# Optimization experiments

Hardware: AMD Instinct MI355X
Metric: run time of the kernel (lower is better)

Reference implementation:

```python
import jax, jax.numpy as jnp
import numpy as np

N_ITERS = 21
TEMPERATURE = 0.01


def setup_inputs() -> dict:
    key = jax.random.key(0)
    input_tensor = jax.random.normal(key, (65536, 1296), dtype=jnp.float32)
    return {"input_tensor": input_tensor}


def reference(input_tensor) -> jnp.ndarray:
    n = input_tensor.shape[1]
    m = n // 36  # 36: side length of the permutation matrix
    log_alpha = input_tensor.reshape(-1, m, m) / TEMPERATURE  # [B, 36, 36]
    # 21 Sinkhorn iterations: alternate row / column log-normalization.
    # Same math as log(sum(exp(.))) in the torch source, written stably.
    for _ in range(N_ITERS):
        log_alpha = log_alpha - jax.nn.logsumexp(log_alpha, axis=2, keepdims=True)
        log_alpha = log_alpha - jax.nn.logsumexp(log_alpha, axis=1, keepdims=True)
    return jnp.exp(log_alpha)
```

## Files before the change

kernel.cpp:

```cpp
#include <hip/hip_runtime.h>

#define SCALE 144.269504088896340736f

template <int CTRL>
__device__ __forceinline__ float dppf(float x) {
    return __builtin_bit_cast(
        float, __builtin_amdgcn_update_dpp(0, __builtin_bit_cast(int, x),
                                           CTRL, 0xF, 0xF, true));
}

__device__ __forceinline__ float qsum(float x) {
    x += dppf<0x39>(x);
    x += dppf<0x4E>(x);
    return x;
}
__device__ __forceinline__ float qmax(float x) {
    x = fmaxf(x, dppf<0x39>(x));
    x = fmaxf(x, dppf<0x4E>(x));
    return x;
}
__device__ __forceinline__ float asum(float x) {
    x += dppf<0x124>(x);
    x += dppf<0x128>(x);
    return x;
}
__device__ __forceinline__ float amax(float x) {
    x = fmaxf(x, dppf<0x124>(x));
    x = fmaxf(x, dppf<0x128>(x));
    return x;
}

typedef float f32x4 __attribute__((ext_vector_type(4)));

__device__ __forceinline__ f32x4 load4u(const float* p) {
    f32x4 v;
    __builtin_memcpy(&v, p, 16);
    return v;
}
__device__ __forceinline__ void store4u(float* p, f32x4 v) {
    __builtin_memcpy(p, &v, 16);
}

__global__ __launch_bounds__(256, 3) void sinkhorn_kernel(
    const float* __restrict__ in, float* __restrict__ out) {
    const int lane = threadIdx.x & 63;
    const int wv   = threadIdx.x >> 6;
    const int q    = lane >> 4;
    const int a    = (lane >> 2) & 3;
    const int b    = lane & 3;
    const int m    = blockIdx.x * 16 + wv * 4 + q;

    const float* src = in  + (size_t)m * 1296 + (a * 9) * 36 + b * 9;
    float*       dst = out + (size_t)m * 1296 + (a * 9) * 36 + b * 9;

    float C[81];
    #pragma unroll
    for (int r = 0; r < 9; ++r) {
        f32x4 v0 = load4u(src + r * 36);
        f32x4 v1 = load4u(src + r * 36 + 4);
        #pragma unroll
        for (int s = 0; s < 4; ++s) C[r * 9 + s] = v0[s];
        #pragma unroll
        for (int s = 0; s < 4; ++s) C[r * 9 + 4 + s] = v1[s];
        C[r * 9 + 8] = src[r * 36 + 8];
    }

    float a2s[9], u[9], w[9];
    #pragma unroll
    for (int r = 0; r < 9; ++r) {
        float mx = C[r * 9];
        #pragma unroll
        for (int s = 1; s < 9; ++s) mx = fmaxf(mx, C[r * 9 + s]);
        a2s[r] = qmax(mx) * SCALE;
    }

    #pragma unroll
    for (int r = 0; r < 9; ++r) {
        float acc = 0.f;
        #pragma unroll
        for (int s = 0; s < 9; ++s)
            acc += __builtin_amdgcn_exp2f(
                __builtin_fmaf(C[r * 9 + s], SCALE, -a2s[r]));
        u[r] = __builtin_amdgcn_rcpf(qsum(acc));
    }

    float b2s[9];
    #pragma unroll
    for (int s = 0; s < 9; ++s) {
        float mx = __builtin_fmaf(C[s], SCALE, -a2s[0]);
        #pragma unroll
        for (int r = 1; r < 9; ++r)
            mx = fmaxf(mx, __builtin_fmaf(C[r * 9 + s], SCALE, -a2s[r]));
        b2s[s] = amax(mx);
    }

    #pragma unroll
    for (int r = 0; r < 9; ++r)
        #pragma unroll
        for (int s = 0; s < 9; ++s)
            C[r * 9 + s] = __builtin_amdgcn_exp2f(
                __builtin_fmaf(C[r * 9 + s], SCALE, -a2s[r]) - b2s[s]);

    #pragma unroll
    for (int s = 0; s < 9; ++s) {
        float acc = 0.f;
        #pragma unroll
        for (int r = 0; r < 9; ++r) acc = fmaf(C[r * 9 + s], u[r], acc);
        w[s] = __builtin_amdgcn_rcpf(asum(acc));
    }

    #pragma unroll 1
    for (int it = 0; it < 20; ++it) {
        #pragma unroll
        for (int r = 0; r < 9; ++r) {
            float acc = 0.f;
            #pragma unroll
            for (int s = 0; s < 9; ++s) acc = fmaf(C[r * 9 + s], w[s], acc);
            u[r] = __builtin_amdgcn_rcpf(qsum(acc));
        }
        #pragma unroll
        for (int s = 0; s < 9; ++s) {
            float acc = 0.f;
            #pragma unroll
            for (int r = 0; r < 9; ++r) acc = fmaf(C[r * 9 + s], u[r], acc);
            w[s] = __builtin_amdgcn_rcpf(asum(acc));
        }
    }

    #pragma unroll
    for (int r = 0; r < 9; ++r) {
        const float ur = u[r];
        float p[9];
        #pragma unroll
        for (int s = 0; s < 9; ++s) p[s] = C[r * 9 + s] * ur * w[s];
        f32x4 v0, v1;
        #pragma unroll
        for (int s = 0; s < 4; ++s) v0[s] = p[s];
        #pragma unroll
        for (int s = 0; s < 4; ++s) v1[s] = p[4 + s];
        store4u(dst + r * 36, v0);
        store4u(dst + r * 36 + 4, v1);
        dst[r * 36 + 8] = p[8];
    }
}

extern "C" void kernel_launch(void* const* d_in, const int* in_sizes, int n_in,
                              void* d_out, int out_size, void* d_ws, size_t ws_size,
                              hipStream_t stream) {
    const float* in  = (const float*)d_in[0];
    float*       out = (float*)d_out;
    sinkhorn_kernel<<<dim3(4096), dim3(256), 0, stream>>>(in, out);
}
```

Measured before the change: 575.8 us.

## Pack Sinkhorn matvecs into float2 ops and reorder initial normalisation

Stores the per-thread 9x9 block as eight float2 columns plus one scalar column so the repeated row and column matvecs can use packed FP32 multiply/FMA (v_pk_fma_f32) on CDNA. The setup is also reordered: the column max is taken first, the kernel is exponentiated once, and the first row normaliser is folded in by scaling with exp2 of the column max. This drops the separate exp pass per row. The risk is extra register pressure or scalarisation if the compiler does not emit packed instructions, and a slightly different numerical path for the first normalisation.

```diff
diff --git a/kernel.cpp b/kernel.cpp
--- a/kernel.cpp
+++ b/kernel.cpp
@@ -1,6 +1,9 @@
 #include <hip/hip_runtime.h>
 
 #define SCALE 144.269504088896340736f
+
+typedef float f32x2 __attribute__((ext_vector_type(2)));
+typedef float f32x4 __attribute__((ext_vector_type(4)));
 
 template <int CTRL>
 __device__ __forceinline__ float dppf(float x) {
@@ -30,8 +33,6 @@
     return x;
 }
 
-typedef float f32x4 __attribute__((ext_vector_type(4)));
-
 __device__ __forceinline__ f32x4 load4u(const float* p) {
     f32x4 v;
     __builtin_memcpy(&v, p, 16);
@@ -53,94 +54,138 @@
     const float* src = in  + (size_t)m * 1296 + (a * 9) * 36 + b * 9;
     float*       dst = out + (size_t)m * 1296 + (a * 9) * 36 + b * 9;
 
-    float C[81];
+    f32x2 C2[9][4];
+    float C8[9];
     #pragma unroll
     for (int r = 0; r < 9; ++r) {
         f32x4 v0 = load4u(src + r * 36);
         f32x4 v1 = load4u(src + r * 36 + 4);
-        #pragma unroll
-        for (int s = 0; s < 4; ++s) C[r * 9 + s] = v0[s];
-        #pragma unroll
-        for (int s = 0; s < 4; ++s) C[r * 9 + 4 + s] = v1[s];
-        C[r * 9 + 8] = src[r * 36 + 8];
+        C2[r][0] = f32x2{v0.x, v0.y};
+        C2[r][1] = f32x2{v0.z, v0.w};
+        C2[r][2] = f32x2{v1.x, v1.y};
+        C2[r][3] = f32x2{v1.z, v1.w};
+        C8[r] = src[r * 36 + 8];
     }
 
-    float a2s[9], u[9], w[9];
+    float a2s[9];
     #pragma unroll
     for (int r = 0; r < 9; ++r) {
-        float mx = C[r * 9];
+        float mx = C8[r];
         #pragma unroll
-        for (int s = 1; s < 9; ++s) mx = fmaxf(mx, C[r * 9 + s]);
+        for (int p = 0; p < 4; ++p)
+            mx = fmaxf(mx, fmaxf(C2[r][p].x, C2[r][p].y));
         a2s[r] = qmax(mx) * SCALE;
+    }
+
+    const f32x2 S2 = {SCALE, SCALE};
+    #pragma unroll
+    for (int r = 0; r < 9; ++r) {
+        const f32x2 a2p = {a2s[r], a2s[r]};
+        #pragma unroll
+        for (int p = 0; p < 4; ++p) C2[r][p] = C2[r][p] * S2 - a2p;
+        C8[r] = __builtin_fmaf(C8[r], SCALE, -a2s[r]);
+    }
+
+    f32x2 b22[4];
+    float b28;
+    #pragma unroll
+    for (int p = 0; p < 4; ++p) {
+        f32x2 mx = C2[0][p];
+        #pragma unroll
+        for (int r = 1; r < 9; ++r) {
+            mx.x = fmaxf(mx.x, C2[r][p].x);
+            mx.y = fmaxf(mx.y, C2[r][p].y);
+        }
+        b22[p] = f32x2{amax(mx.x), amax(mx.y)};
+    }
+    {
+        float mx = C8[0];
+        #pragma unroll
+        for (int r = 1; r < 9; ++r) mx = fmaxf(mx, C8[r]);
+        b28 = amax(mx);
     }
 
     #pragma unroll
     for (int r = 0; r < 9; ++r) {
-        float acc = 0.f;
         #pragma unroll
-        for (int s = 0; s < 9; ++s)
-            acc += __builtin_amdgcn_exp2f(
-                __builtin_fmaf(C[r * 9 + s], SCALE, -a2s[r]));
-        u[r] = __builtin_amdgcn_rcpf(qsum(acc));
+        for (int p = 0; p < 4; ++p) {
+            const f32x2 e = C2[r][p] - b22[p];
+            C2[r][p].x = __builtin_amdgcn_exp2f(e.x);
+            C2[r][p].y = __builtin_amdgcn_exp2f(e.y);
+        }
+        C8[r] = __builtin_amdgcn_exp2f(C8[r] - b28);
     }
 
-    float b2s[9];
-    #pragma unroll
-    for (int s = 0; s < 9; ++s) {
-        float mx = __builtin_fmaf(C[s], SCALE, -a2s[0]);
+    f32x2 u2[9];
+    {
+        f32x2 t2[4];
         #pragma unroll
-        for (int r = 1; r < 9; ++r)
-            mx = fmaxf(mx, __builtin_fmaf(C[r * 9 + s], SCALE, -a2s[r]));
-        b2s[s] = amax(mx);
+        for (int p = 0; p < 4; ++p)
+            t2[p] = f32x2{__builtin_amdgcn_exp2f(b22[p].x),
+                          __builtin_amdgcn_exp2f(b22[p].y)};
+        const float t8 = __builtin_amdgcn_exp2f(b28);
+        #pragma unroll
+        for (int r = 0; r < 9; ++r) {
+            f32x2 acc2 = C2[r][0] * t2[0];
+            #pragma unroll
+            for (int p = 1; p < 4; ++p) acc2 += C2[r][p] * t2[p];
+            const float acc = __builtin_fmaf(C8[r], t8, acc2.x) + acc2.y;
+            const float ur = __builtin_amdgcn_rcpf(qsum(acc));
+            u2[r] = f32x2{ur, ur};
+        }
     }
 
-    #pragma unroll
-    for (int r = 0; r < 9; ++r)
+    f32x2 w2[4];
+    float w8;
+
+    auto col_step = [&]() {
+        f32x2 acc[4];
         #pragma unroll
-        for (int s = 0; s < 9; ++s)
-            C[r * 9 + s] = __builtin_amdgcn_exp2f(
-                __builtin_fmaf(C[r * 9 + s], SCALE, -a2s[r]) - b2s[s]);
+        for (int p = 0; p < 4; ++p) acc[p] = C2[0][p] * u2[0];
+        float acc8 = C8[0] * u2[0].x;
+        #pragma unroll
+        for (int r = 1; r < 9; ++r) {
+            #pragma unroll
+            for (int p = 0; p < 4; ++p) acc[p] += C2[r][p] * u2[r];
+            acc8 = __builtin_fmaf(C8[r], u2[r].x, acc8);
+        }
+        #pragma unroll
+        for (int p = 0; p < 4; ++p)
+            w2[p] = f32x2{__builtin_amdgcn_rcpf(asum(acc[p].x)),
+                          __builtin_amdgcn_rcpf(asum(acc[p].y))};
+        w8 = __builtin_amdgcn_rcpf(asum(acc8));
+    };
 
-    #pragma unroll
-    for (int s = 0; s < 9; ++s) {
-        float acc = 0.f;
+    auto row_step = [&]() {
         #pragma unroll
-        for (int r = 0; r < 9; ++r) acc = fmaf(C[r * 9 + s], u[r], acc);
-        w[s] = __builtin_amdgcn_rcpf(asum(acc));
-    }
+        for (int r = 0; r < 9; ++r) {
+            f32x2 acc2 = C2[r][0] * w2[0];
+            #pragma unroll
+            for (int p = 1; p < 4; ++p) acc2 += C2[r][p] * w2[p];
+            const float acc = __builtin_fmaf(C8[r], w8, acc2.x) + acc2.y;
+            const float ur = __builtin_amdgcn_rcpf(qsum(acc));
+            u2[r] = f32x2{ur, ur};
+        }
+    };
+
+    col_step();
 
     #pragma unroll 1
     for (int it = 0; it < 20; ++it) {
-        #pragma unroll
-        for (int r = 0; r < 9; ++r) {
-            float acc = 0.f;
-            #pragma unroll
-            for (int s = 0; s < 9; ++s) acc = fmaf(C[r * 9 + s], w[s], acc);
-            u[r] = __builtin_amdgcn_rcpf(qsum(acc));
-        }
-        #pragma unroll
-        for (int s = 0; s < 9; ++s) {
-            float acc = 0.f;
-            #pragma unroll
-            for (int r = 0; r < 9; ++r) acc = fmaf(C[r * 9 + s], u[r], acc);
-            w[s] = __builtin_amdgcn_rcpf(asum(acc));
-        }
+        row_step();
+        col_step();
     }
 
     #pragma unroll
     for (int r = 0; r < 9; ++r) {
-        const float ur = u[r];
-        float p[9];
-        #pragma unroll
-        for (int s = 0; s < 9; ++s) p[s] = C[r * 9 + s] * ur * w[s];
-        f32x4 v0, v1;
-        #pragma unroll
-        for (int s = 0; s < 4; ++s) v0[s] = p[s];
-        #pragma unroll
-        for (int s = 0; s < 4; ++s) v1[s] = p[4 + s];
-        store4u(dst + r * 36, v0);
-        store4u(dst + r * 36 + 4, v1);
-        dst[r * 36 + 8] = p[8];
+        const f32x2 uu = u2[r];
+        const f32x2 t0 = C2[r][0] * uu * w2[0];
+        const f32x2 t1 = C2[r][1] * uu * w2[1];
+        const f32x2 t2_ = C2[r][2] * uu * w2[2];
+        const f32x2 t3 = C2[r][3] * uu * w2[3];
+        store4u(dst + r * 36, f32x4{t0.x, t0.y, t1.x, t1.y});
+        store4u(dst + r * 36 + 4, f32x4{t2_.x, t2_.y, t3.x, t3.y});
+        dst[r * 36 + 8] = C8[r] * uu.x * w8;
     }
 }
 
```

After: 571.8 us. Within noise of the previous version (-0.7%).
